# Optimization experiments

Measured on AMD Instinct MI355X. Metric: run time of the kernel, lower is better.

Reference implementation:

```python
import jax, jax.numpy as jnp
import numpy as np

N_OUT = 4096
N_IN = 4096
N_SPARSE = 1024  # int(0.25 * N_IN)
BATCH, SEQ = 4, 2048


def setup_inputs() -> dict:
    key = jax.random.key(0)
    k1, k2, k3 = jax.random.split(key, 3)
    x = jax.random.normal(k1, (BATCH, SEQ, N_IN), dtype=jnp.float32)
    sparse_values = jax.random.normal(k2, (N_OUT, N_SPARSE), dtype=jnp.float32)
    # static equivalent of the boolean sparse_mask: sorted unique column indices
    sparse_idx = jnp.sort(jax.random.permutation(k3, N_IN)[:N_SPARSE]).astype(jnp.int64)
    return {"x": x, "sparse_values": sparse_values, "sparse_idx": sparse_idx}


def reference(x, sparse_values, sparse_idx):
    # x[..., mask] @ sparse_values.T  ->  gather columns then GEMM
    x_g = jnp.take(x, sparse_idx, axis=-1)          # [B, S, n_sparse]
    return jnp.einsum('bsk,ok->bso', x_g, sparse_values)  # [B, S, n_out]
```

## Files before the change

### kernel.cpp

```cpp
#include <hip/hip_runtime.h>
#include <hip/hip_bf16.h>

#define NOUT  4096
#define KDIM  1024
#define MROWS 8192

typedef __attribute__((ext_vector_type(8))) short bf16x8;
typedef __attribute__((ext_vector_type(4))) float f32x4;

__device__ __forceinline__ unsigned short f2bf(float f) {
  union { float f; unsigned int u; } c; c.f = f;
  unsigned int lsb = (c.u >> 16) & 1u;
  c.u += 0x7fffu + lsb;
  return (unsigned short)(c.u >> 16);
}

__device__ __forceinline__ void gload_lds16(const void* g, void* l) {
  __builtin_amdgcn_global_load_lds(
      (const __attribute__((address_space(1))) void*)g,
      (__attribute__((address_space(3))) void*)l, 16, 0, 0);
}

#define FENCE() asm volatile("" ::: "memory")
#define BAR() do { FENCE(); __builtin_amdgcn_s_barrier(); FENCE(); } while (0)
#define VMW(n) asm volatile("s_waitcnt vmcnt(" #n ")" ::: "memory")

__global__ __launch_bounds__(256) void gather_x(const float* __restrict__ x,
                                                const void* __restrict__ idx_raw,
                                                unsigned short* __restrict__ xg) {
  __shared__ float row[NOUT == 0 ? 1 : 4096];
  __shared__ int sidx[1024];
  const long long* p64 = (const long long*)idx_raw;
  const int* p32 = (const int*)idx_raw;
  const bool is64 = ((unsigned long long)p64[0]) < 4096ull;
  const int t = threadIdx.x;
  const int m = blockIdx.x;
  const float* src = x + (size_t)m * 4096;
#pragma unroll
  for (int i = 0; i < 4; ++i)
    ((float4*)row)[t + 256 * i] = ((const float4*)src)[t + 256 * i];
  if (is64) {
#pragma unroll
    for (int i = 0; i < 4; ++i) sidx[t + 256 * i] = (int)p64[t + 256 * i];
  } else {
#pragma unroll
    for (int i = 0; i < 4; ++i) sidx[t + 256 * i] = p32[t + 256 * i];
  }
  __syncthreads();
  unsigned short* dst = xg + (size_t)m * 1024;
#pragma unroll
  for (int i = 0; i < 4; ++i) {
    int k = t + 256 * i;
    dst[k] = f2bf(row[sidx[k]]);
  }
}

__global__ __launch_bounds__(256) void cvt_w(const float* __restrict__ w,
                                             unsigned short* __restrict__ wb) {
  const int i = blockIdx.x * 256 + threadIdx.x;
  float4 v = ((const float4*)w)[i];
  ushort4 o;
  o.x = f2bf(v.x); o.y = f2bf(v.y); o.z = f2bf(v.z); o.w = f2bf(v.w);
  ((ushort4*)wb)[i] = o;
}

__global__ __launch_bounds__(512, 2) void gemm256(const unsigned short* __restrict__ A,
                                                  const unsigned short* __restrict__ B,
                                                  float* __restrict__ C) {
  __shared__ __align__(16) unsigned short lds[65536];

  const int tid = threadIdx.x;
  const int lane = tid & 63;
  const int wid = tid >> 6;
  const int wm = wid >> 2, wn = wid & 3;
  const int l15 = lane & 15, lq = lane >> 4;
  const int swz = l15 & 7;

  const int bn0 = blockIdx.x * 256;
  const int bm0 = blockIdx.y * 256;

  const int r0 = tid >> 3;
  const int cg = (tid & 7) ^ (r0 & 7);
  const unsigned short* Ag = A + (size_t)(bm0 + r0) * KDIM + cg * 8;
  const unsigned short* Bg = B + (size_t)(bn0 + r0) * KDIM + cg * 8;
  const int tid8 = tid * 8;

  const int cA0 = (lq ^ swz) * 8;
  const int cA1 = cA0 ^ 32;
  const int aOff = wm * 8192 + l15 * 64;
  const int bOff = 32768 + (wn >> 1) * 8192 + (wn & 1) * 4096 + l15 * 64;

  f32x4 acc[8][4] = {};
  bf16x8 a0[4], a1[4], bA0[2], bA1[2], bB0[2], bB1[2];

#define LOAD_A(D, MH) do {                                                       \
    const unsigned short* _p = lds + (D) * 16384 + aOff + (MH) * 4096;           \
    a0[0] = *(const bf16x8*)(_p + cA0);        a1[0] = *(const bf16x8*)(_p + cA1);        \
    a0[1] = *(const bf16x8*)(_p + 1024 + cA0); a1[1] = *(const bf16x8*)(_p + 1024 + cA1); \
    a0[2] = *(const bf16x8*)(_p + 2048 + cA0); a1[2] = *(const bf16x8*)(_p + 2048 + cA1); \
    a0[3] = *(const bf16x8*)(_p + 3072 + cA0); a1[3] = *(const bf16x8*)(_p + 3072 + cA1); \
  } while (0)

#define LOAD_B(D, NH, B0, B1) do {                                               \
    const unsigned short* _p = lds + (D) * 16384 + bOff + (NH) * 2048;           \
    B0[0] = *(const bf16x8*)(_p + cA0);        B1[0] = *(const bf16x8*)(_p + cA1);        \
    B0[1] = *(const bf16x8*)(_p + 1024 + cA0); B1[1] = *(const bf16x8*)(_p + 1024 + cA1); \
  } while (0)

#define STAGE_A(D, T, H) do {                                                                  \
    gload_lds16(Ag + (size_t)((H) * 128) * KDIM + (T) * 64,                                    \
                lds + (D) * 16384 + (H) * 8192 + tid8);                                        \
    gload_lds16(Ag + (size_t)((H) * 128 + 64) * KDIM + (T) * 64,                               \
                lds + (D) * 16384 + (H) * 8192 + 4096 + tid8);                                 \
  } while (0)

#define STAGE_B(D, T, H) do {                                                                  \
    gload_lds16(Bg + (size_t)((H) * 128) * KDIM + (T) * 64,                                    \
                lds + 32768 + (D) * 16384 + (H) * 8192 + tid8);                                \
    gload_lds16(Bg + (size_t)((H) * 128 + 64) * KDIM + (T) * 64,                               \
                lds + 32768 + (D) * 16384 + (H) * 8192 + 4096 + tid8);                         \
  } while (0)

#define MFMA_Q(MH, NH, B0, B1) do {                                                            \
    __builtin_amdgcn_s_setprio(1);                                                             \
    _Pragma("unroll") for (int mf = 0; mf < 4; ++mf) {                                         \
      _Pragma("unroll") for (int nf = 0; nf < 2; ++nf) {                                       \
        acc[(MH)*4+mf][(NH)*2+nf] = __builtin_amdgcn_mfma_f32_16x16x32_bf16(                   \
            a0[mf], B0[nf], acc[(MH)*4+mf][(NH)*2+nf], 0, 0, 0);                               \
        acc[(MH)*4+mf][(NH)*2+nf] = __builtin_amdgcn_mfma_f32_16x16x32_bf16(                   \
            a1[mf], B1[nf], acc[(MH)*4+mf][(NH)*2+nf], 0, 0, 0);                               \
      }                                                                                        \
    }                                                                                          \
    __builtin_amdgcn_s_setprio(0);                                                             \
  } while (0)

  STAGE_B(0, 0, 0); STAGE_B(0, 0, 1);
  STAGE_A(0, 0, 0); STAGE_A(0, 0, 1);
  STAGE_B(1, 1, 0); STAGE_B(1, 1, 1);
  VMW(4);
  BAR();

  for (int i = 0; i < 8; ++i) {
    const int tA1 = 2 * i + 1;
    const int tN0 = (2 * i + 2) & 15;
    const int tN1 = (2 * i + 3) & 15;

    LOAD_A(0, 0); LOAD_B(0, 0, bA0, bA1); STAGE_A(1, tA1, 0);
    BAR(); MFMA_Q(0, 0, bA0, bA1); BAR();
    LOAD_B(0, 1, bB0, bB1); STAGE_A(1, tA1, 1);
    BAR(); MFMA_Q(0, 1, bB0, bB1); BAR();
    LOAD_A(0, 1); STAGE_B(0, tN0, 0);
    BAR(); MFMA_Q(1, 0, bA0, bA1); BAR();
    STAGE_B(0, tN0, 1);
    BAR(); MFMA_Q(1, 1, bB0, bB1); VMW(4); BAR();
    LOAD_A(1, 0); LOAD_B(1, 0, bA0, bA1); STAGE_A(0, tN0, 0);
    BAR(); MFMA_Q(0, 0, bA0, bA1); BAR();
    LOAD_B(1, 1, bB0, bB1); STAGE_A(0, tN0, 1);
    BAR(); MFMA_Q(0, 1, bB0, bB1); BAR();
    LOAD_A(1, 1); STAGE_B(1, tN1, 0);
    BAR(); MFMA_Q(1, 0, bA0, bA1); BAR();
    STAGE_B(1, tN1, 1);
    BAR(); MFMA_Q(1, 1, bB0, bB1); VMW(4); BAR();
  }

  VMW(0);
  float* Crow = C + (size_t)(bm0 + wm * 128 + lq * 4) * NOUT + bn0 + wn * 64 + l15;
#pragma unroll
  for (int mf = 0; mf < 8; ++mf)
#pragma unroll
    for (int nf = 0; nf < 4; ++nf)
#pragma unroll
      for (int j = 0; j < 4; ++j)
        Crow[(size_t)(mf * 16 + j) * NOUT + nf * 16] = acc[mf][nf][j];

#undef LOAD_A
#undef LOAD_B
#undef STAGE_A
#undef STAGE_B
#undef MFMA_Q
}

extern "C" void kernel_launch(void* const* d_in, const int* in_sizes, int n_in,
                              void* d_out, int out_size, void* d_ws, size_t ws_size,
                              hipStream_t stream) {
  const float* x   = (const float*)d_in[0];
  const float* sv  = (const float*)d_in[1];
  const void*  idx = d_in[2];
  float* out = (float*)d_out;

  unsigned short* xg = (unsigned short*)d_ws;
  unsigned short* wb = xg + (size_t)MROWS * KDIM;

  gather_x<<<MROWS, 256, 0, stream>>>(x, idx, xg);
  cvt_w<<<(NOUT * KDIM / 4) / 256, 256, 0, stream>>>(sv, wb);

  dim3 grid(NOUT / 256, MROWS / 256);
  gemm256<<<grid, 512, 0, stream>>>(xg, wb, out);
}
```

Before: 111.8 us.

## Switch GEMM to 32x32x16 MFMA and fuse gather and weight conversion kernels

The GEMM inner loop now issues 32x32x16 bf16 MFMAs with 32-row fragments in place of 16x16x32, which changes the LDS read pattern, the register fragment layout and the output store mapping. The aim is fewer MFMA issues and LDS reads per unit of work. Separately, the gather-to-bf16 and weight-to-bf16 kernels are merged into one launch, with 4 rows per block and vectorized ushort4 stores. This saves one launch and improves store width, at the cost of more LDS use per prep block.

```diff
diff --git a/kernel.cpp b/kernel.cpp
--- a/kernel.cpp
+++ b/kernel.cpp
@@ -6,7 +6,7 @@
 #define MROWS 8192
 
 typedef __attribute__((ext_vector_type(8))) short bf16x8;
-typedef __attribute__((ext_vector_type(4))) float f32x4;
+typedef __attribute__((ext_vector_type(16))) float f32x16;
 
 __device__ __forceinline__ unsigned short f2bf(float f) {
   union { float f; unsigned int u; } c; c.f = f;
@@ -25,43 +25,56 @@
 #define BAR() do { FENCE(); __builtin_amdgcn_s_barrier(); FENCE(); } while (0)
 #define VMW(n) asm volatile("s_waitcnt vmcnt(" #n ")" ::: "memory")
 
-__global__ __launch_bounds__(256) void gather_x(const float* __restrict__ x,
-                                                const void* __restrict__ idx_raw,
-                                                unsigned short* __restrict__ xg) {
-  __shared__ float row[NOUT == 0 ? 1 : 4096];
+__global__ __launch_bounds__(512) void prep(const float* __restrict__ x,
+                                            const void* __restrict__ idx_raw,
+                                            const float* __restrict__ w,
+                                            unsigned short* __restrict__ xg,
+                                            unsigned short* __restrict__ wb) {
+  __shared__ float rows[16384];
   __shared__ int sidx[1024];
-  const long long* p64 = (const long long*)idx_raw;
-  const int* p32 = (const int*)idx_raw;
-  const bool is64 = ((unsigned long long)p64[0]) < 4096ull;
+  const int b = blockIdx.x;
   const int t = threadIdx.x;
-  const int m = blockIdx.x;
-  const float* src = x + (size_t)m * 4096;
-#pragma unroll
-  for (int i = 0; i < 4; ++i)
-    ((float4*)row)[t + 256 * i] = ((const float4*)src)[t + 256 * i];
-  if (is64) {
-#pragma unroll
-    for (int i = 0; i < 4; ++i) sidx[t + 256 * i] = (int)p64[t + 256 * i];
+
+  if (b < 2048) {
+    const long long* p64 = (const long long*)idx_raw;
+    const int* p32 = (const int*)idx_raw;
+    const bool is64 = ((unsigned long long)p64[0]) < 4096ull;
+    const float* src = x + (size_t)b * 4 * 4096;
+#pragma unroll
+    for (int i = 0; i < 8; ++i)
+      ((float4*)rows)[t + 512 * i] = ((const float4*)src)[t + 512 * i];
+    if (is64) {
+      sidx[t] = (int)p64[t];
+      sidx[t + 512] = (int)p64[t + 512];
+    } else {
+      sidx[t] = p32[t];
+      sidx[t + 512] = p32[t + 512];
+    }
+    __syncthreads();
+    ushort4* dst = (ushort4*)(xg + (size_t)b * 4 * 1024);
+#pragma unroll
+    for (int i = 0; i < 2; ++i) {
+      const int q = t + 512 * i;
+      const int e = 4 * q;
+      const int rbase = (e >> 10) * 4096;
+      const int k = e & 1023;
+      ushort4 o;
+      o.x = f2bf(rows[rbase + sidx[k + 0]]);
+      o.y = f2bf(rows[rbase + sidx[k + 1]]);
+      o.z = f2bf(rows[rbase + sidx[k + 2]]);
+      o.w = f2bf(rows[rbase + sidx[k + 3]]);
+      dst[q] = o;
+    }
   } else {
-#pragma unroll
-    for (int i = 0; i < 4; ++i) sidx[t + 256 * i] = p32[t + 256 * i];
+    const int i0 = (b - 2048) * 2048 + t;
+#pragma unroll
+    for (int j = 0; j < 4; ++j) {
+      float4 v = ((const float4*)w)[i0 + 512 * j];
+      ushort4 o;
+      o.x = f2bf(v.x); o.y = f2bf(v.y); o.z = f2bf(v.z); o.w = f2bf(v.w);
+      ((ushort4*)wb)[i0 + 512 * j] = o;
+    }
   }
-  __syncthreads();
-  unsigned short* dst = xg + (size_t)m * 1024;
-#pragma unroll
-  for (int i = 0; i < 4; ++i) {
-    int k = t + 256 * i;
-    dst[k] = f2bf(row[sidx[k]]);
-  }
-}
-
-__global__ __launch_bounds__(256) void cvt_w(const float* __restrict__ w,
-                                             unsigned short* __restrict__ wb) {
-  const int i = blockIdx.x * 256 + threadIdx.x;
-  float4 v = ((const float4*)w)[i];
-  ushort4 o;
-  o.x = f2bf(v.x); o.y = f2bf(v.y); o.z = f2bf(v.z); o.w = f2bf(v.w);
-  ((ushort4*)wb)[i] = o;
 }
 
 __global__ __launch_bounds__(512, 2) void gemm256(const unsigned short* __restrict__ A,
@@ -73,65 +86,65 @@
   const int lane = tid & 63;
   const int wid = tid >> 6;
   const int wm = wid >> 2, wn = wid & 3;
-  const int l15 = lane & 15, lq = lane >> 4;
-  const int swz = l15 & 7;
+  const int l31 = lane & 31, lh = lane >> 5;
+  const int sw = l31 & 7;
 
   const int bn0 = blockIdx.x * 256;
   const int bm0 = blockIdx.y * 256;
 
-  const int r0 = tid >> 3;
-  const int cg = (tid & 7) ^ (r0 & 7);
-  const unsigned short* Ag = A + (size_t)(bm0 + r0) * KDIM + cg * 8;
-  const unsigned short* Bg = B + (size_t)(bn0 + r0) * KDIM + cg * 8;
+  const int pr = tid >> 3;
+  const int cg = (tid & 7) ^ (pr & 7);
+  const unsigned short* Ag = A + (size_t)(bm0 + pr) * KDIM + cg * 8;
+  const unsigned short* Bg = B + (size_t)(bn0 + pr) * KDIM + cg * 8;
   const int tid8 = tid * 8;
 
-  const int cA0 = (lq ^ swz) * 8;
-  const int cA1 = cA0 ^ 32;
-  const int aOff = wm * 8192 + l15 * 64;
-  const int bOff = 32768 + (wn >> 1) * 8192 + (wn & 1) * 4096 + l15 * 64;
-
-  f32x4 acc[8][4] = {};
-  bf16x8 a0[4], a1[4], bA0[2], bA1[2], bB0[2], bB1[2];
-
-#define LOAD_A(D, MH) do {                                                       \
-    const unsigned short* _p = lds + (D) * 16384 + aOff + (MH) * 4096;           \
-    a0[0] = *(const bf16x8*)(_p + cA0);        a1[0] = *(const bf16x8*)(_p + cA1);        \
-    a0[1] = *(const bf16x8*)(_p + 1024 + cA0); a1[1] = *(const bf16x8*)(_p + 1024 + cA1); \
-    a0[2] = *(const bf16x8*)(_p + 2048 + cA0); a1[2] = *(const bf16x8*)(_p + 2048 + cA1); \
-    a0[3] = *(const bf16x8*)(_p + 3072 + cA0); a1[3] = *(const bf16x8*)(_p + 3072 + cA1); \
-  } while (0)
-
-#define LOAD_B(D, NH, B0, B1) do {                                               \
-    const unsigned short* _p = lds + (D) * 16384 + bOff + (NH) * 2048;           \
-    B0[0] = *(const bf16x8*)(_p + cA0);        B1[0] = *(const bf16x8*)(_p + cA1);        \
-    B0[1] = *(const bf16x8*)(_p + 1024 + cA0); B1[1] = *(const bf16x8*)(_p + 1024 + cA1); \
-  } while (0)
-
-#define STAGE_A(D, T, H) do {                                                                  \
-    gload_lds16(Ag + (size_t)((H) * 128) * KDIM + (T) * 64,                                    \
-                lds + (D) * 16384 + (H) * 8192 + tid8);                                        \
-    gload_lds16(Ag + (size_t)((H) * 128 + 64) * KDIM + (T) * 64,                               \
-                lds + (D) * 16384 + (H) * 8192 + 4096 + tid8);                                 \
-  } while (0)
-
-#define STAGE_B(D, T, H) do {                                                                  \
-    gload_lds16(Bg + (size_t)((H) * 128) * KDIM + (T) * 64,                                    \
-                lds + 32768 + (D) * 16384 + (H) * 8192 + tid8);                                \
-    gload_lds16(Bg + (size_t)((H) * 128 + 64) * KDIM + (T) * 64,                               \
-                lds + 32768 + (D) * 16384 + (H) * 8192 + 4096 + tid8);                         \
-  } while (0)
-
-#define MFMA_Q(MH, NH, B0, B1) do {                                                            \
-    __builtin_amdgcn_s_setprio(1);                                                             \
-    _Pragma("unroll") for (int mf = 0; mf < 4; ++mf) {                                         \
-      _Pragma("unroll") for (int nf = 0; nf < 2; ++nf) {                                       \
-        acc[(MH)*4+mf][(NH)*2+nf] = __builtin_amdgcn_mfma_f32_16x16x32_bf16(                   \
-            a0[mf], B0[nf], acc[(MH)*4+mf][(NH)*2+nf], 0, 0, 0);                               \
-        acc[(MH)*4+mf][(NH)*2+nf] = __builtin_amdgcn_mfma_f32_16x16x32_bf16(                   \
-            a1[mf], B1[nf], acc[(MH)*4+mf][(NH)*2+nf], 0, 0, 0);                               \
-      }                                                                                        \
-    }                                                                                          \
-    __builtin_amdgcn_s_setprio(0);                                                             \
+  const int cK0 = ((0 + lh) ^ sw) * 8;
+  const int cK1 = ((2 + lh) ^ sw) * 8;
+  const int cK2 = ((4 + lh) ^ sw) * 8;
+  const int cK3 = ((6 + lh) ^ sw) * 8;
+  const int aRow = wm * 8192 + l31 * 64;
+  const int bRow = 32768 + wn * 4096 + l31 * 64;
+
+  f32x16 acc[4][2] = {};
+  bf16x8 a[2][4], bN0[4], bN1[4];
+
+#define LOAD_A(D, MH) do {                                                        \
+    const unsigned short* _p = lds + (D) * 16384 + aRow + (MH) * 4096;            \
+    a[0][0] = *(const bf16x8*)(_p + cK0);        a[0][1] = *(const bf16x8*)(_p + cK1);         \
+    a[0][2] = *(const bf16x8*)(_p + cK2);        a[0][3] = *(const bf16x8*)(_p + cK3);         \
+    a[1][0] = *(const bf16x8*)(_p + 2048 + cK0); a[1][1] = *(const bf16x8*)(_p + 2048 + cK1);  \
+    a[1][2] = *(const bf16x8*)(_p + 2048 + cK2); a[1][3] = *(const bf16x8*)(_p + 2048 + cK3);  \
+  } while (0)
+
+#define LOAD_B(D, NF, R) do {                                                     \
+    const unsigned short* _p = lds + (D) * 16384 + bRow + (NF) * 2048;            \
+    R[0] = *(const bf16x8*)(_p + cK0); R[1] = *(const bf16x8*)(_p + cK1);         \
+    R[2] = *(const bf16x8*)(_p + cK2); R[3] = *(const bf16x8*)(_p + cK3);         \
+  } while (0)
+
+#define STAGE_A(D, T, H) do {                                                     \
+    gload_lds16(Ag + (size_t)((H) * 128) * KDIM + (T) * 64,                       \
+                lds + (D) * 16384 + (H) * 8192 + tid8);                           \
+    gload_lds16(Ag + (size_t)((H) * 128 + 64) * KDIM + (T) * 64,                  \
+                lds + (D) * 16384 + (H) * 8192 + 4096 + tid8);                    \
+  } while (0)
+
+#define STAGE_B(D, T, H) do {                                                     \
+    gload_lds16(Bg + (size_t)((H) * 128) * KDIM + (T) * 64,                       \
+                lds + 32768 + (D) * 16384 + (H) * 8192 + tid8);                   \
+    gload_lds16(Bg + (size_t)((H) * 128 + 64) * KDIM + (T) * 64,                  \
+                lds + 32768 + (D) * 16384 + (H) * 8192 + 4096 + tid8);            \
+  } while (0)
+
+#define MFMA_Q(MH, NH, R) do {                                                    \
+    __builtin_amdgcn_s_setprio(1);                                                \
+    _Pragma("unroll") for (int kb = 0; kb < 4; ++kb) {                            \
+      _Pragma("unroll") for (int mf = 0; mf < 2; ++mf) {                          \
+        acc[(MH)*2+mf][NH] = __builtin_amdgcn_mfma_f32_32x32x16_bf16(             \
+            a[mf][kb], R[kb], acc[(MH)*2+mf][NH], 0, 0, 0);                       \
+      }                                                                           \
+    }                                                                             \
+    __builtin_amdgcn_s_setprio(0);                                                \
   } while (0)
 
   STAGE_B(0, 0, 0); STAGE_B(0, 0, 1);
@@ -145,33 +158,37 @@
     const int tN0 = (2 * i + 2) & 15;
     const int tN1 = (2 * i + 3) & 15;
 
-    LOAD_A(0, 0); LOAD_B(0, 0, bA0, bA1); STAGE_A(1, tA1, 0);
-    BAR(); MFMA_Q(0, 0, bA0, bA1); BAR();
-    LOAD_B(0, 1, bB0, bB1); STAGE_A(1, tA1, 1);
-    BAR(); MFMA_Q(0, 1, bB0, bB1); BAR();
+    LOAD_A(0, 0); LOAD_B(0, 0, bN0); STAGE_A(1, tA1, 0);
+    BAR(); MFMA_Q(0, 0, bN0); BAR();
+    LOAD_B(0, 1, bN1); STAGE_A(1, tA1, 1);
+    BAR(); MFMA_Q(0, 1, bN1); BAR();
     LOAD_A(0, 1); STAGE_B(0, tN0, 0);
-    BAR(); MFMA_Q(1, 0, bA0, bA1); BAR();
+    BAR(); MFMA_Q(1, 0, bN0); BAR();
     STAGE_B(0, tN0, 1);
-    BAR(); MFMA_Q(1, 1, bB0, bB1); VMW(4); BAR();
-    LOAD_A(1, 0); LOAD_B(1, 0, bA0, bA1); STAGE_A(0, tN0, 0);
-    BAR(); MFMA_Q(0, 0, bA0, bA1); BAR();
-    LOAD_B(1, 1, bB0, bB1); STAGE_A(0, tN0, 1);
-    BAR(); MFMA_Q(0, 1, bB0, bB1); BAR();
+    BAR(); MFMA_Q(1, 1, bN1); VMW(4); BAR();
+    LOAD_A(1, 0); LOAD_B(1, 0, bN0); STAGE_A(0, tN0, 0);
+    BAR(); MFMA_Q(0, 0, bN0); BAR();
+    LOAD_B(1, 1, bN1); STAGE_A(0, tN0, 1);
+    BAR(); MFMA_Q(0, 1, bN1); BAR();
     LOAD_A(1, 1); STAGE_B(1, tN1, 0);
-    BAR(); MFMA_Q(1, 0, bA0, bA1); BAR();
+    BAR(); MFMA_Q(1, 0, bN0); BAR();
     STAGE_B(1, tN1, 1);
-    BAR(); MFMA_Q(1, 1, bB0, bB1); VMW(4); BAR();
+    BAR(); MFMA_Q(1, 1, bN1); VMW(4); BAR();
   }
 
   VMW(0);
-  float* Crow = C + (size_t)(bm0 + wm * 128 + lq * 4) * NOUT + bn0 + wn * 64 + l15;
-#pragma unroll
-  for (int mf = 0; mf < 8; ++mf)
-#pragma unroll
-    for (int nf = 0; nf < 4; ++nf)
-#pragma unroll
-      for (int j = 0; j < 4; ++j)
-        Crow[(size_t)(mf * 16 + j) * NOUT + nf * 16] = acc[mf][nf][j];
+  float* base = C + (size_t)(bm0 + wm * 128) * NOUT + bn0 + wn * 64;
+#pragma unroll
+  for (int mf = 0; mf < 4; ++mf)
+#pragma unroll
+    for (int nf = 0; nf < 2; ++nf) {
+      f32x16 v = acc[mf][nf];
+#pragma unroll
+      for (int r = 0; r < 16; ++r) {
+        const int rowi = mf * 32 + (r & 3) + 8 * (r >> 2) + 4 * lh;
+        base[(size_t)rowi * NOUT + nf * 32 + l31] = v[r];
+      }
+    }
 
 #undef LOAD_A
 #undef LOAD_B
@@ -191,8 +208,7 @@
   unsigned short* xg = (unsigned short*)d_ws;
   unsigned short* wb = xg + (size_t)MROWS * KDIM;
 
-  gather_x<<<MROWS, 256, 0, stream>>>(x, idx, xg);
-  cvt_w<<<(NOUT * KDIM / 4) / 256, 256, 0, stream>>>(sv, wb);
+  prep<<<2560, 512, 0, stream>>>(x, idx, sv, xg, wb);
 
   dim3 grid(NOUT / 256, MROWS / 256);
   gemm256<<<grid, 512, 0, stream>>>(xg, wb, out);
```

Result: slower. 119.2 us (+6.6%).
